# Kernel tuning notes

Measured on AMD Instinct MI355X. Metric: run time of the kernel, lower is better.

## Reference

```python
import jax, jax.numpy as jnp
import numpy as np

NUM_HEADS = 12

def setup_inputs() -> dict:
    key = jax.random.key(0)
    k1, k2 = jax.random.split(key)
    X = jax.random.normal(k1, (2, 2048, 768), dtype=jnp.float32)
    # torch nn.Linear(dim, 2*dim, bias=False) weight has shape [2*dim, dim]
    W_qkv = jax.random.normal(k2, (1536, 768), dtype=jnp.float32) * (768 ** -0.5)
    return {"X": X, "W_qkv": W_qkv}

def reference(X, W_qkv):
    B, N, C = X.shape
    H = NUM_HEADS
    hd = C // H
    scale = hd ** -0.5
    # qkv: [B, N, 2, H, hd]
    qkv = (X @ W_qkv.T).reshape(B, N, 2, H, hd)
    q = jnp.transpose(qkv[:, :, 0], (0, 2, 1, 3))  # [B, H, N, hd]
    k = jnp.transpose(qkv[:, :, 1], (0, 2, 1, 3))  # [B, H, N, hd]
    attn = jnp.einsum('bhnd,bhmd->bhnm', q, k) * scale  # [B, H, N, N]
    # dropout p=0 -> identity; double sum over heads and keys
    scores = attn.sum(axis=1).sum(axis=-1)  # [B, N]
    return scores
```

## Files before the change

kernel.cpp:

```cpp
#include <hip/hip_runtime.h>


#define DIM 768
#define BATCH 2
#define SEQ 2048


__global__ void colsum_kernel(const float* __restrict__ X, float* __restrict__ xsum) {
    const int NSPLIT = 32;
    int bx = blockIdx.x;
    int b = bx / (3 * NSPLIT);
    int rem = bx % (3 * NSPLIT);
    int dchunk = rem % 3;
    int nchunk = rem / 3;
    int d = dchunk * 256 + threadIdx.x;
    const float* base = X + (size_t)b * SEQ * DIM + (size_t)nchunk * (SEQ / NSPLIT) * DIM + d;
    float acc = 0.f;
    #pragma unroll 8
    for (int n = 0; n < SEQ / NSPLIT; ++n)
        acc += base[(size_t)n * DIM];
    atomicAdd(&xsum[b * DIM + d], acc);
}

__global__ void kv_matvec_kernel(const float* __restrict__ W, const float* __restrict__ xsum,
                                 float* __restrict__ v) {
    int w = blockIdx.x * 4 + (threadIdx.x >> 6);
    int lane = threadIdx.x & 63;
    int b = w / DIM;
    int c = w % DIM;
    const float4* wrow = (const float4*)(W + (size_t)(DIM + c) * DIM);
    const float4* xs   = (const float4*)(xsum + b * DIM);
    float acc = 0.f;
    #pragma unroll
    for (int j = 0; j < 3; ++j) {
        float4 a = wrow[lane + 64 * j];
        float4 s = xs[lane + 64 * j];
        acc += a.x * s.x + a.y * s.y + a.z * s.z + a.w * s.w;
    }
    #pragma unroll
    for (int off = 32; off > 0; off >>= 1)
        acc += __shfl_down(acc, off, 64);
    if (lane == 0) v[b * DIM + c] = acc;
}

__global__ void wq_t_matvec_kernel(const float* __restrict__ W, const float* __restrict__ v,
                                   float* __restrict__ t) {
    const int CSPLIT = 8;
    int bx = blockIdx.x;
    int b = bx / (3 * CSPLIT);
    int rem = bx % (3 * CSPLIT);
    int dchunk = rem % 3;
    int cchunk = rem / 3;
    int d = dchunk * 256 + threadIdx.x;
    const float* vb = v + b * DIM;
    float acc = 0.f;
    int c0 = cchunk * (DIM / CSPLIT);
    #pragma unroll 8
    for (int c = c0; c < c0 + DIM / CSPLIT; ++c)
        acc += W[(size_t)c * DIM + d] * vb[c];
    atomicAdd(&t[b * DIM + d], acc);
}

__global__ void scores_kernel(const float* __restrict__ X, const float* __restrict__ t,
                              float* __restrict__ out) {
    int r = blockIdx.x * 4 + (threadIdx.x >> 6);
    int lane = threadIdx.x & 63;
    int b = r >> 11;
    const float4* xr = (const float4*)(X + (size_t)r * DIM);
    const float4* tb = (const float4*)(t + b * DIM);
    float acc = 0.f;
    #pragma unroll
    for (int j = 0; j < 3; ++j) {
        float4 a = xr[lane + 64 * j];
        float4 s = tb[lane + 64 * j];
        acc += a.x * s.x + a.y * s.y + a.z * s.z + a.w * s.w;
    }
    #pragma unroll
    for (int off = 32; off > 0; off >>= 1)
        acc += __shfl_down(acc, off, 64);
    if (lane == 0) out[r] = 0.125f * acc;
}

extern "C" void kernel_launch(void* const* d_in, const int* in_sizes, int n_in,
                              void* d_out, int out_size, void* d_ws, size_t ws_size,
                              hipStream_t stream) {
    const float* X = (const float*)d_in[0];
    const float* W = (const float*)d_in[1];
    float* out = (float*)d_out;
    float* ws = (float*)d_ws;
    float* xsum = ws;
    float* v    = ws + 2 * DIM;
    float* t    = ws + 4 * DIM;

    hipMemsetAsync(d_ws, 0, 6 * DIM * sizeof(float), stream);

    colsum_kernel<<<BATCH * 3 * 32, 256, 0, stream>>>(X, xsum);
    kv_matvec_kernel<<<BATCH * DIM / 4, 256, 0, stream>>>(W, xsum, v);
    wq_t_matvec_kernel<<<BATCH * 3 * 8, 256, 0, stream>>>(W, v, t);
    scores_kernel<<<BATCH * SEQ / 4, 256, 0, stream>>>(X, t, out);
}
```

Baseline: 78.33 us.

## Replace atomics and memset with partial-sum buffers reduced in consumer kernels

Removes the workspace memset and all atomicAdd reductions. Column sums and t partials are now written to per-chunk buffers and reduced inside the next kernel through shared memory. Column sums use float4 loads over 64 chunks, and the v kernel computes four outputs per wave. This saves one launch and the atomic traffic, but every consumer block repeats the partial reduction, which costs extra reads.

```diff
diff --git a/kernel.cpp b/kernel.cpp
--- a/kernel.cpp
+++ b/kernel.cpp
@@ -6,79 +6,105 @@
 #define SEQ 2048
 
 
-__global__ void colsum_kernel(const float* __restrict__ X, float* __restrict__ xsum) {
-    const int NSPLIT = 32;
-    int bx = blockIdx.x;
-    int b = bx / (3 * NSPLIT);
-    int rem = bx % (3 * NSPLIT);
-    int dchunk = rem % 3;
-    int nchunk = rem / 3;
-    int d = dchunk * 256 + threadIdx.x;
-    const float* base = X + (size_t)b * SEQ * DIM + (size_t)nchunk * (SEQ / NSPLIT) * DIM + d;
-    float acc = 0.f;
+__global__ void colsum_part(const float* __restrict__ X, float* __restrict__ part) {
+    int b  = blockIdx.x >> 6;
+    int ch = blockIdx.x & 63;
+    int i  = threadIdx.x;
+    const float4* base = (const float4*)(X + ((size_t)b * SEQ + (size_t)ch * 32) * DIM) + i;
+    float4 a = {0.f, 0.f, 0.f, 0.f};
     #pragma unroll 8
-    for (int n = 0; n < SEQ / NSPLIT; ++n)
-        acc += base[(size_t)n * DIM];
-    atomicAdd(&xsum[b * DIM + d], acc);
+    for (int n = 0; n < 32; ++n) {
+        float4 x = base[n * 192];
+        a.x += x.x; a.y += x.y; a.z += x.z; a.w += x.w;
+    }
+    ((float4*)(part + (size_t)(b * 64 + ch) * DIM))[i] = a;
 }
 
-__global__ void kv_matvec_kernel(const float* __restrict__ W, const float* __restrict__ xsum,
-                                 float* __restrict__ v) {
-    int w = blockIdx.x * 4 + (threadIdx.x >> 6);
-    int lane = threadIdx.x & 63;
-    int b = w / DIM;
-    int c = w % DIM;
-    const float4* wrow = (const float4*)(W + (size_t)(DIM + c) * DIM);
-    const float4* xs   = (const float4*)(xsum + b * DIM);
-    float acc = 0.f;
+__global__ void v_kernel(const float* __restrict__ W, const float* __restrict__ part,
+                         float* __restrict__ v) {
+    __shared__ alignas(16) float xs[DIM];
+    int bi = blockIdx.x;
+    int b = bi >= 48;
+    int tid = threadIdx.x;
+    for (int d = tid; d < DIM; d += 256) {
+        float s = 0.f;
+        #pragma unroll 8
+        for (int ch = 0; ch < 64; ++ch)
+            s += part[(size_t)(b * 64 + ch) * DIM + d];
+        xs[d] = s;
+    }
+    __syncthreads();
+    int gw = bi * 4 + (tid >> 6);
+    int lane = tid & 63;
+    const float4* xs4 = (const float4*)xs;
     #pragma unroll
-    for (int j = 0; j < 3; ++j) {
-        float4 a = wrow[lane + 64 * j];
-        float4 s = xs[lane + 64 * j];
-        acc += a.x * s.x + a.y * s.y + a.z * s.z + a.w * s.w;
+    for (int k = 0; k < 4; ++k) {
+        int o = gw * 4 + k;
+        int c = o - b * DIM;
+        const float4* wr = (const float4*)(W + (size_t)(DIM + c) * DIM);
+        float acc = 0.f;
+        #pragma unroll
+        for (int j = 0; j < 3; ++j) {
+            float4 a = wr[lane + 64 * j];
+            float4 s = xs4[lane + 64 * j];
+            acc += a.x * s.x + a.y * s.y + a.z * s.z + a.w * s.w;
+        }
+        #pragma unroll
+        for (int off = 32; off; off >>= 1)
+            acc += __shfl_down(acc, off, 64);
+        if (lane == 0) v[o] = acc;
     }
-    #pragma unroll
-    for (int off = 32; off > 0; off >>= 1)
-        acc += __shfl_down(acc, off, 64);
-    if (lane == 0) v[b * DIM + c] = acc;
 }
 
-__global__ void wq_t_matvec_kernel(const float* __restrict__ W, const float* __restrict__ v,
-                                   float* __restrict__ t) {
-    const int CSPLIT = 8;
-    int bx = blockIdx.x;
-    int b = bx / (3 * CSPLIT);
-    int rem = bx % (3 * CSPLIT);
-    int dchunk = rem % 3;
-    int cchunk = rem / 3;
-    int d = dchunk * 256 + threadIdx.x;
+__global__ void t_part(const float* __restrict__ W, const float* __restrict__ v,
+                       float* __restrict__ tp) {
+    int bi = blockIdx.x;
+    int b = bi / 24;
+    int rem = bi % 24;
+    int cs = rem / 3;
+    int dch = rem % 3;
+    int d = dch * 256 + threadIdx.x;
     const float* vb = v + b * DIM;
     float acc = 0.f;
-    int c0 = cchunk * (DIM / CSPLIT);
+    int c0 = cs * 96;
     #pragma unroll 8
-    for (int c = c0; c < c0 + DIM / CSPLIT; ++c)
+    for (int c = c0; c < c0 + 96; ++c)
         acc += W[(size_t)c * DIM + d] * vb[c];
-    atomicAdd(&t[b * DIM + d], acc);
+    tp[(size_t)(b * 8 + cs) * DIM + d] = acc;
 }
 
-__global__ void scores_kernel(const float* __restrict__ X, const float* __restrict__ t,
-                              float* __restrict__ out) {
-    int r = blockIdx.x * 4 + (threadIdx.x >> 6);
-    int lane = threadIdx.x & 63;
-    int b = r >> 11;
+__global__ void scores_k(const float* __restrict__ X, const float* __restrict__ tp,
+                         float* __restrict__ out) {
+    __shared__ alignas(16) float ft[DIM];
+    int r0 = blockIdx.x * 4;
+    int b = r0 >> 11;
+    int tid = threadIdx.x;
+    if (tid < 192) {
+        const float4* base = (const float4*)(tp + (size_t)b * 8 * DIM) + tid;
+        float4 s = {0.f, 0.f, 0.f, 0.f};
+        #pragma unroll
+        for (int cs = 0; cs < 8; ++cs) {
+            float4 a = base[cs * 192];
+            s.x += a.x; s.y += a.y; s.z += a.z; s.w += a.w;
+        }
+        ((float4*)ft)[tid] = s;
+    }
+    __syncthreads();
+    int r = r0 + (tid >> 6);
+    int lane = tid & 63;
     const float4* xr = (const float4*)(X + (size_t)r * DIM);
-    const float4* tb = (const float4*)(t + b * DIM);
+    const float4* t4 = (const float4*)ft;
     float acc = 0.f;
     #pragma unroll
     for (int j = 0; j < 3; ++j) {
         float4 a = xr[lane + 64 * j];
-        float4 s = tb[lane + 64 * j];
+        float4 s = t4[lane + 64 * j];
         acc += a.x * s.x + a.y * s.y + a.z * s.z + a.w * s.w;
     }
     #pragma unroll
-    for (int off = 32; off > 0; off >>= 1)
+    for (int off = 32; off; off >>= 1)
         acc += __shfl_down(acc, off, 64);
-    if (lane == 0) out[r] = 0.125f * acc;
+    if (lane == 0) out[r] = acc * 0.125f;
 }
 
 extern "C" void kernel_launch(void* const* d_in, const int* in_sizes, int n_in,
@@ -88,14 +114,12 @@
     const float* W = (const float*)d_in[1];
     float* out = (float*)d_out;
     float* ws = (float*)d_ws;
-    float* xsum = ws;
-    float* v    = ws + 2 * DIM;
-    float* t    = ws + 4 * DIM;
+    float* part = ws;
+    float* v    = ws + 2 * 64 * DIM;
+    float* tp   = v + 2 * DIM;
 
-    hipMemsetAsync(d_ws, 0, 6 * DIM * sizeof(float), stream);
-
-    colsum_kernel<<<BATCH * 3 * 32, 256, 0, stream>>>(X, xsum);
-    kv_matvec_kernel<<<BATCH * DIM / 4, 256, 0, stream>>>(W, xsum, v);
-    wq_t_matvec_kernel<<<BATCH * 3 * 8, 256, 0, stream>>>(W, v, t);
-    scores_kernel<<<BATCH * SEQ / 4, 256, 0, stream>>>(X, t, out);
+    colsum_part<<<128, 192, 0, stream>>>(X, part);
+    v_kernel  <<<96, 256, 0, stream>>>(W, part, v);
+    t_part    <<<48, 256, 0, stream>>>(W, v, tp);
+    scores_k  <<<1024, 256, 0, stream>>>(X, tp, out);
 }
```

Measured after the change: 86.44 us. 1.1x slower.
